# Performance work log

Hardware: AMD Instinct MI355X
Metric: run time of the kernel (lower is better)

The kernel has to match this reference:

```python
import jax, jax.numpy as jnp
import numpy as np

INPUT_DIM = 1024
OUTPUT_DIM = 1024
NUM_HEADS = 16  # NOTE: torch .split(num_heads) => chunk SIZE = num_heads
N_CHUNKS = OUTPUT_DIM // NUM_HEADS  # 64 effective heads of dim 16
NEG_INF = -1e9


def setup_inputs() -> dict:
    key = jax.random.key(0)
    k1, k2, k3, k4 = jax.random.split(key, 4)
    B, S = 32, 256
    x = jax.random.normal(k1, (B, S, INPUT_DIM), dtype=jnp.float32)
    mask = jnp.ones((B, S), dtype=jnp.float32)
    # xavier-uniform-ish linear weights, torch layout [out, in]
    lim = float(np.sqrt(6.0 / (INPUT_DIM + OUTPUT_DIM)))
    Wq = jax.random.uniform(k2, (OUTPUT_DIM, INPUT_DIM), jnp.float32, -lim, lim)
    Wk = jax.random.uniform(k3, (OUTPUT_DIM, INPUT_DIM), jnp.float32, -lim, lim)
    Wv = jax.random.uniform(k4, (OUTPUT_DIM, INPUT_DIM), jnp.float32, -lim, lim)
    return {"batch_sequence": x, "sequence_mask": mask, "Wq": Wq, "Wk": Wk, "Wv": Wv}


def _split_heads(m):
    # [B,S,D] -> chunks of size NUM_HEADS stacked in dim 0: [C,B,S,H]
    B, S, D = m.shape
    return jnp.transpose(m.reshape(B, S, N_CHUNKS, NUM_HEADS), (2, 0, 1, 3))


def reference(batch_sequence, sequence_mask, Wq, Wk, Wv):
    q = _split_heads(batch_sequence @ Wq.T)  # [C,B,S,H]
    k = _split_heads(batch_sequence @ Wk.T)
    v = _split_heads(batch_sequence @ Wv.T)
    logits = jnp.einsum("cbqh,cbkh->cbqk", q, k) / jnp.sqrt(
        jnp.asarray(OUTPUT_DIM, batch_sequence.dtype)
    )
    mask2d = sequence_mask[:, :, None] * sequence_mask[:, None, :]  # [B,S,S]
    logits = jnp.where(mask2d[None] > 0, logits, NEG_INF)
    w = jax.nn.softmax(logits, axis=-1)
    out = jnp.einsum("cbqk,cbkh->cbqh", w, v)  # [C,B,S,H]
    B, S = batch_sequence.shape[:2]
    return jnp.transpose(out, (1, 2, 0, 3)).reshape(B, S, OUTPUT_DIM)
```

## Files before the change

### kernel.cpp

```cpp
#include <hip/hip_runtime.h>


typedef unsigned short u16;
typedef unsigned int u32;
typedef __attribute__((ext_vector_type(8))) short short8;
typedef __attribute__((ext_vector_type(4))) short short4v;
typedef __attribute__((ext_vector_type(4))) float floatx4;

#if __has_builtin(__builtin_amdgcn_mfma_f32_16x16x16bf16_1k)
#define MFMA16(A, B, C) __builtin_amdgcn_mfma_f32_16x16x16bf16_1k(A, B, C, 0, 0, 0)
#elif __has_builtin(__builtin_amdgcn_mfma_f32_16x16x16_bf16)
#define MFMA16(A, B, C) __builtin_amdgcn_mfma_f32_16x16x16_bf16(A, B, C, 0, 0, 0)
#else
__device__ __forceinline__ floatx4 mfma16_asm(short4v a, short4v b, floatx4 c) {
  floatx4 d;
  asm volatile("v_mfma_f32_16x16x16_bf16 %0, %1, %2, %3"
               : "=v"(d) : "v"(a), "v"(b), "v"(c));
  return d;
}
#define MFMA16(A, B, C) mfma16_asm(A, B, C)
#endif

__device__ __forceinline__ u16 f2bf(float f) {
  union { float f; u32 u; } x; x.f = f;
  u32 r = x.u + 0x7fffu + ((x.u >> 16) & 1u);
  return (u16)(r >> 16);
}
__device__ __forceinline__ float bf2f(u16 u) {
  union { u32 u; float f; } x; x.u = ((u32)u) << 16;
  return x.f;
}

__device__ __forceinline__ void gload16(const void* g, void* l) {
  typedef __attribute__((address_space(1))) const unsigned int gq;
  typedef __attribute__((address_space(3))) unsigned int lq;
  __builtin_amdgcn_global_load_lds((gq*)(size_t)g, (lq*)(size_t)l, 16, 0, 0);
}

#define GM 8192
#define GN 3072
#define GK 1024
#define CSTR 136
#define QKVSEG (64 * 32 * 4096)

__global__ __launch_bounds__(256) void cast_all(const float* __restrict__ x,
                                                const float* __restrict__ wq,
                                                const float* __restrict__ wk,
                                                const float* __restrict__ wv,
                                                u16* __restrict__ XB,
                                                u16* __restrict__ WB) {
  int bid = blockIdx.x;
  const float* src; u16* dst; int off;
  if (bid < 8192)       { src = x;  dst = XB;                 off = bid; }
  else if (bid < 9216)  { src = wq; dst = WB;                 off = bid - 8192; }
  else if (bid < 10240) { src = wk; dst = WB + 1024 * 1024;   off = bid - 9216; }
  else                  { src = wv; dst = WB + 2 * 1024 * 1024; off = bid - 10240; }
  int i = (off * 256 + threadIdx.x) * 4;
  float4 v = *(const float4*)(src + i);
  u32 lo = (u32)f2bf(v.x) | ((u32)f2bf(v.y) << 16);
  u32 hi = (u32)f2bf(v.z) | ((u32)f2bf(v.w) << 16);
  uint2 o; o.x = lo; o.y = hi;
  *(uint2*)(dst + i) = o;
}

__global__ __launch_bounds__(256) void gemm_qkv(const u16* __restrict__ A,
                                                const u16* __restrict__ B,
                                                u16* __restrict__ QKV) {
  __shared__ u16 smem[17408];
  u16* As = smem;
  u16* Bs = smem + 128 * 64;

  const int t = threadIdx.x;
  const int lid = blockIdx.x;
  const int xcd = lid & 7;
  const int slot = lid >> 3;
  const int m0 = (xcd * 8 + (slot & 7)) * 128;
  const int n0 = (slot >> 3) * 128;

  const int wave = t >> 6;
  const int lane = t & 63;
  const int wm = (wave >> 1) * 64;
  const int wn = (wave & 1) * 64;
  const int lrow = lane & 15;
  const int quad = lane >> 4;

  const int r_loc = lane >> 3;
  const int xb = (lane & 7) ^ r_loc;

  floatx4 acc[4][4] = {};

  const size_t arow = (size_t)(m0 + wave * 32 + r_loc) * GK + xb * 8;
  const size_t brow = (size_t)(n0 + wave * 32 + r_loc) * GK + xb * 8;

  for (int k0 = 0; k0 < GK; k0 += 64) {
    __syncthreads();
#pragma unroll
    for (int i = 0; i < 4; i++) {
      gload16(A + arow + (size_t)i * 8 * GK + k0, As + (wave * 32 + i * 8) * 64);
      gload16(B + brow + (size_t)i * 8 * GK + k0, Bs + (wave * 32 + i * 8) * 64);
    }
    __syncthreads();
#pragma unroll
    for (int kk = 0; kk < 2; kk++) {
      short8 af[4], bf[4];
#pragma unroll
      for (int i = 0; i < 4; i++) {
        int row = wm + i * 16 + lrow;
        int pos = ((kk * 4 + quad) ^ (lane & 7)) * 8;
        af[i] = *(const short8*)(As + row * 64 + pos);
      }
#pragma unroll
      for (int j = 0; j < 4; j++) {
        int row = wn + j * 16 + lrow;
        int pos = ((kk * 4 + quad) ^ (lane & 7)) * 8;
        bf[j] = *(const short8*)(Bs + row * 64 + pos);
      }
#pragma unroll
      for (int i = 0; i < 4; i++)
#pragma unroll
        for (int j = 0; j < 4; j++)
          acc[i][j] = __builtin_amdgcn_mfma_f32_16x16x32_bf16(af[i], bf[j], acc[i][j], 0, 0, 0);
    }
  }

  __syncthreads();
  u16* Cs = smem;

  const int crow0 = quad * 4;
  const int ccol = lane & 15;
#pragma unroll
  for (int i = 0; i < 4; i++)
#pragma unroll
    for (int j = 0; j < 4; j++)
#pragma unroll
      for (int r = 0; r < 4; r++)
        Cs[(wm + i * 16 + crow0 + r) * CSTR + wn + j * 16 + ccol] = f2bf(acc[i][j][r]);
  __syncthreads();

  const int qkv = n0 >> 10;
  const int c0 = (n0 >> 4) & 63;
  const int b = m0 >> 8;
  const int s0 = m0 & 255;
  const int s = t >> 1;
  const int hh = (t & 1) * 8;

#pragma unroll
  for (int g = 0; g < 8; g++) {
    uint4 val = *(const uint4*)(Cs + s * CSTR + g * 16 + hh);
    size_t base = (((size_t)(qkv * 64 + c0 + g) * 32 + b) * 256 + (s0 + s)) * 16 + hh;
    *(uint4*)(QKV + base) = val;
  }
}

__global__ __launch_bounds__(256) void attn_kernel(const u16* __restrict__ QKV,
                                                   const float* __restrict__ mask,
                                                   float* __restrict__ out) {
  __shared__ float m_s[256];
  __shared__ float l_s[256];
  __shared__ float ot[16 * 257];

  const int c = blockIdx.x;
  const int b = blockIdx.y;
  const int t = threadIdx.x;
  const int wave = t >> 6;
  const int lane = t & 63;
  const int col = lane & 15;
  const int quad = lane >> 4;

  const size_t hb = ((size_t)c * 32 + b) * 4096;
  const u16* Qp = QKV + hb;
  const u16* Kp = QKV + QKVSEG + hb;
  const u16* Vp = QKV + 2 * QKVSEG + hb;

  m_s[t] = mask[b * 256 + t];
  __syncthreads();

  const int q0 = wave * 64;

  short4v bq[4];
#pragma unroll
  for (int qt = 0; qt < 4; qt++)
    bq[qt] = *(const short4v*)(Qp + (q0 + qt * 16 + col) * 16 + quad * 4);

  float mqv[4];
#pragma unroll
  for (int qt = 0; qt < 4; qt++) mqv[qt] = m_s[q0 + qt * 16 + col];

  floatx4 oacc[4] = {};
  float lsum[4] = {0.f, 0.f, 0.f, 0.f};

  for (int kt = 0; kt < 16; kt++) {
    const int kb = kt * 16;
    short4v ak = *(const short4v*)(Kp + (kb + col) * 16 + quad * 4);
    short4v av;
#pragma unroll
    for (int i = 0; i < 4; i++)
      av[i] = (short)Vp[(kb + quad * 4 + i) * 16 + col];
    float mk[4];
#pragma unroll
    for (int i = 0; i < 4; i++) mk[i] = m_s[kb + quad * 4 + i];

#pragma unroll
    for (int qt = 0; qt < 4; qt++) {
      floatx4 z = {0.f, 0.f, 0.f, 0.f};
      floatx4 st = MFMA16(ak, bq[qt], z);
      short4v p;
      float ps = 0.f;
#pragma unroll
      for (int i = 0; i < 4; i++) {
        float e = __expf(st[i] * 0.03125f);
        e = (mqv[qt] * mk[i] > 0.f) ? e : 0.f;
        u16 pb = f2bf(e);
        p[i] = (short)pb;
        ps += bf2f(pb);
      }
      lsum[qt] += ps;
      oacc[qt] = MFMA16(av, p, oacc[qt]);
    }
  }

#pragma unroll
  for (int qt = 0; qt < 4; qt++) {
    float l = lsum[qt];
    l += __shfl_xor(l, 16, 64);
    l += __shfl_xor(l, 32, 64);
    if (quad == 0) l_s[q0 + qt * 16 + col] = l;
#pragma unroll
    for (int r = 0; r < 4; r++)
      ot[(quad * 4 + r) * 257 + q0 + qt * 16 + col] = oacc[qt][r];
  }
  __syncthreads();

  float l = l_s[t];
  float* op = out + ((size_t)b * 256 + t) * 1024 + c * 16;
  float o[16];
  if (l > 0.f) {
    float inv = 1.0f / l;
#pragma unroll
    for (int h = 0; h < 16; h++) o[h] = ot[h * 257 + t] * inv;
  } else {
#pragma unroll
    for (int h = 0; h < 16; h++) o[h] = 0.f;
    for (int k = 0; k < 256; k++)
#pragma unroll
      for (int h = 0; h < 16; h++) o[h] += bf2f(Vp[k * 16 + h]);
#pragma unroll
    for (int h = 0; h < 16; h++) o[h] *= (1.0f / 256.0f);
  }
#pragma unroll
  for (int g = 0; g < 4; g++) {
    float4 r;
    r.x = o[g * 4 + 0]; r.y = o[g * 4 + 1]; r.z = o[g * 4 + 2]; r.w = o[g * 4 + 3];
    *(float4*)(op + g * 4) = r;
  }
}

extern "C" void kernel_launch(void* const* d_in, const int* in_sizes, int n_in,
                              void* d_out, int out_size, void* d_ws, size_t ws_size,
                              hipStream_t stream) {
  const float* x    = (const float*)d_in[0];
  const float* mask = (const float*)d_in[1];
  const float* Wq   = (const float*)d_in[2];
  const float* Wk   = (const float*)d_in[3];
  const float* Wv   = (const float*)d_in[4];
  float* out = (float*)d_out;

  u16* XB  = (u16*)d_ws;
  u16* WB  = XB + (size_t)GM * GK;
  u16* QKV = WB + (size_t)GN * GK;

  cast_all<<<11264, 256, 0, stream>>>(x, Wq, Wk, Wv, XB, WB);
  gemm_qkv<<<1536, 256, 0, stream>>>(XB, WB, QKV);
  attn_kernel<<<dim3(64, 32), 256, 0, stream>>>(QKV, mask, out);
}
```

Measured before the change: 201.3 us.

## Fold softmax scale into Q, use exp2, MFMA row sums, fast path for all-ones mask

Folds the 1/sqrt(D)*log2(e) scale into Q in the GEMM epilogue so attention can call a raw exp2. Replaces the scalar bf16 round-trip row-sum with an MFMA against a ones vector, and truncates to bf16 via byte permute instead of round-to-nearest. A block-wide vote on the mask picks an unmasked loop variant that skips the per-element mask test. This trims VALU work in the attention inner loop, but adds bf16 rounding of the pre-scaled Q and coarser truncation of probabilities.

```diff
diff --git a/kernel.cpp b/kernel.cpp
--- a/kernel.cpp
+++ b/kernel.cpp
@@ -20,6 +20,14 @@
 }
 #define MFMA16(A, B, C) mfma16_asm(A, B, C)
 #endif
+
+#if __has_builtin(__builtin_amdgcn_exp2f)
+#define EXP2(x) __builtin_amdgcn_exp2f(x)
+#else
+#define EXP2(x) __expf((x) * 0.6931471805599453f)
+#endif
+
+#define QSCALE 0.045084220f
 
 __device__ __forceinline__ u16 f2bf(float f) {
   union { float f; u32 u; } x; x.f = f;
@@ -126,6 +134,8 @@
   __syncthreads();
   u16* Cs = smem;
 
+  const float qsc = (n0 < 1024) ? QSCALE : 1.0f;
+
   const int crow0 = quad * 4;
   const int ccol = lane & 15;
 #pragma unroll
@@ -134,7 +144,7 @@
     for (int j = 0; j < 4; j++)
 #pragma unroll
       for (int r = 0; r < 4; r++)
-        Cs[(wm + i * 16 + crow0 + r) * CSTR + wn + j * 16 + ccol] = f2bf(acc[i][j][r]);
+        Cs[(wm + i * 16 + crow0 + r) * CSTR + wn + j * 16 + ccol] = f2bf(acc[i][j][r] * qsc);
   __syncthreads();
 
   const int qkv = n0 >> 10;
@@ -149,6 +159,46 @@
     uint4 val = *(const uint4*)(Cs + s * CSTR + g * 16 + hh);
     size_t base = (((size_t)(qkv * 64 + c0 + g) * 32 + b) * 256 + (s0 + s)) * 16 + hh;
     *(uint4*)(QKV + base) = val;
+  }
+}
+
+template <bool MASKED>
+__device__ __forceinline__ void attn_loop(const u16* __restrict__ Kp,
+                                          const u16* __restrict__ Vp,
+                                          const short4v* bq, const float* mqv,
+                                          const float* m_s,
+                                          floatx4* oacc, floatx4* lacc,
+                                          int col, int quad) {
+  const short4v ones = {(short)0x3F80, (short)0x3F80, (short)0x3F80, (short)0x3F80};
+#pragma unroll 2
+  for (int kt = 0; kt < 16; kt++) {
+    const int kb = kt * 16;
+    short4v ak = *(const short4v*)(Kp + (kb + col) * 16 + quad * 4);
+    short4v av;
+#pragma unroll
+    for (int i = 0; i < 4; i++)
+      av[i] = (short)Vp[(kb + quad * 4 + i) * 16 + col];
+    float mk[4];
+    if (MASKED) {
+#pragma unroll
+      for (int i = 0; i < 4; i++) mk[i] = m_s[kb + quad * 4 + i];
+    }
+#pragma unroll
+    for (int qt = 0; qt < 4; qt++) {
+      floatx4 z = {0.f, 0.f, 0.f, 0.f};
+      floatx4 st = MFMA16(ak, bq[qt], z);
+      float e[4];
+#pragma unroll
+      for (int i = 0; i < 4; i++) {
+        e[i] = EXP2(st[i]);
+        if (MASKED) e[i] = (mqv[qt] * mk[i] > 0.f) ? e[i] : 0.f;
+      }
+      union { u32 u[2]; short4v s; } pk;
+      pk.u[0] = __builtin_amdgcn_perm(__float_as_uint(e[1]), __float_as_uint(e[0]), 0x07060302u);
+      pk.u[1] = __builtin_amdgcn_perm(__float_as_uint(e[3]), __float_as_uint(e[2]), 0x07060302u);
+      lacc[qt] = MFMA16(ones, pk.s, lacc[qt]);
+      oacc[qt] = MFMA16(av, pk.s, oacc[qt]);
+    }
   }
 }
 
@@ -172,8 +222,9 @@
   const u16* Kp = QKV + QKVSEG + hb;
   const u16* Vp = QKV + 2 * QKVSEG + hb;
 
-  m_s[t] = mask[b * 256 + t];
-  __syncthreads();
+  float mv = mask[b * 256 + t];
+  m_s[t] = mv;
+  const int allones = __syncthreads_and(mv > 0.f);
 
   const int q0 = wave * 64;
 
@@ -187,44 +238,16 @@
   for (int qt = 0; qt < 4; qt++) mqv[qt] = m_s[q0 + qt * 16 + col];
 
   floatx4 oacc[4] = {};
-  float lsum[4] = {0.f, 0.f, 0.f, 0.f};
-
-  for (int kt = 0; kt < 16; kt++) {
-    const int kb = kt * 16;
-    short4v ak = *(const short4v*)(Kp + (kb + col) * 16 + quad * 4);
-    short4v av;
-#pragma unroll
-    for (int i = 0; i < 4; i++)
-      av[i] = (short)Vp[(kb + quad * 4 + i) * 16 + col];
-    float mk[4];
-#pragma unroll
-    for (int i = 0; i < 4; i++) mk[i] = m_s[kb + quad * 4 + i];
-
-#pragma unroll
-    for (int qt = 0; qt < 4; qt++) {
-      floatx4 z = {0.f, 0.f, 0.f, 0.f};
-      floatx4 st = MFMA16(ak, bq[qt], z);
-      short4v p;
-      float ps = 0.f;
-#pragma unroll
-      for (int i = 0; i < 4; i++) {
-        float e = __expf(st[i] * 0.03125f);
-        e = (mqv[qt] * mk[i] > 0.f) ? e : 0.f;
-        u16 pb = f2bf(e);
-        p[i] = (short)pb;
-        ps += bf2f(pb);
-      }
-      lsum[qt] += ps;
-      oacc[qt] = MFMA16(av, p, oacc[qt]);
-    }
-  }
+  floatx4 lacc[4] = {};
+
+  if (allones)
+    attn_loop<false>(Kp, Vp, bq, mqv, m_s, oacc, lacc, col, quad);
+  else
+    attn_loop<true>(Kp, Vp, bq, mqv, m_s, oacc, lacc, col, quad);
 
 #pragma unroll
   for (int qt = 0; qt < 4; qt++) {
-    float l = lsum[qt];
-    l += __shfl_xor(l, 16, 64);
-    l += __shfl_xor(l, 32, 64);
-    if (quad == 0) l_s[q0 + qt * 16 + col] = l;
+    if (quad == 0) l_s[q0 + qt * 16 + col] = lacc[qt][0];
 #pragma unroll
     for (int r = 0; r < 4; r++)
       ot[(quad * 4 + r) * 257 + q0 + qt * 16 + col] = oacc[qt][r];
@@ -234,7 +257,7 @@
   float l = l_s[t];
   float* op = out + ((size_t)b * 256 + t) * 1024 + c * 16;
   float o[16];
-  if (l > 0.f) {
+  if (allones || l > 0.f) {
     float inv = 1.0f / l;
 #pragma unroll
     for (int h = 0; h < 16; h++) o[h] = ot[h * 257 + t] * inv;
```

New measurement: 187.5 us. 6.8% less time.
